# Performance work log

Hardware: AMD Instinct MI355X
Metric: run time of the kernel (lower is better)

The kernel has to match this reference:

```python
import jax, jax.numpy as jnp
import numpy as np

TOP_K_PCT = 0.1
MAX_SHARP_TOKENS = 10
SMOOTHING = 0.1


def setup_inputs() -> dict:
    key = jax.random.key(0)
    logits = jax.random.normal(key, (2, 8, 2048, 2048), dtype=jnp.float32)
    return {"logits": logits, "dim": 3}


def reference(logits, dim):
    # Move the softmax axis to the end so lax.top_k / row-scatter apply.
    x = jnp.moveaxis(logits, dim, -1)
    N = x.shape[-1]
    k = min(MAX_SHARP_TOKENS, max(1, int(N * TOP_K_PCT)))

    vals, idx = jax.lax.top_k(x, k)            # [..., k], sorted descending
    topk_soft = jax.nn.softmax(vals, axis=-1)  # softmax over just the top-k values

    flat = x.reshape(-1, N)                    # [R, N]
    fidx = idx.reshape(-1, k)                  # [R, k]
    rows = jnp.arange(flat.shape[0])[:, None]

    # boolean mask of top-k positions
    mask = jnp.zeros(flat.shape, dtype=bool).at[rows, fidx].set(True)

    # softmax over the remaining (non-top-k) logits; top-k filled with dtype min
    neg_inf = jnp.finfo(flat.dtype).min
    remaining = jnp.where(mask, neg_inf, flat)
    rem_soft = jax.nn.softmax(remaining, axis=-1)
    rem_soft = jnp.where(mask, jnp.zeros((), flat.dtype), rem_soft)

    # scatter top-k softmax back, then blend
    final = jnp.zeros_like(flat).at[rows, fidx].set(topk_soft.reshape(-1, k))
    out = final * (1.0 - SMOOTHING) + rem_soft * SMOOTHING

    return jnp.moveaxis(out.reshape(x.shape), -1, dim)
```

## Files before the change

### kernel.cpp

```cpp
#include <hip/hip_runtime.h>
#include <math.h>

#define ROW_N 2048
#define KSEL 10
#define WCAP 64

typedef float f32x4 __attribute__((ext_vector_type(4)));
typedef unsigned long long u64;

__global__ __launch_bounds__(256) void topk_softmax_kernel(
    const float* __restrict__ in, float* __restrict__ out)
{
    const int lane = threadIdx.x & 63;
    const int wave = threadIdx.x >> 6;
    const size_t base = ((size_t)blockIdx.x * 4 + wave) * ROW_N;

    __shared__ u64 s_cand[4][WCAP];

    const f32x4* p4 = reinterpret_cast<const f32x4*>(in + base);
    f32x4 V[8];
    #pragma unroll
    for (int j = 0; j < 8; ++j) V[j] = p4[j * 64 + lane];

    const float K = 1.4426950408889634f;
    float m1 = -INFINITY, m2 = -INFINITY, tot0 = 0.f;
    #pragma unroll
    for (int j = 0; j < 8; ++j)
        #pragma unroll
        for (int c = 0; c < 4; ++c) {
            float x = V[j][c];
            m2 = fmaxf(fminf(x, m1), m2);
            m1 = fmaxf(x, m1);
            tot0 += exp2f(x * K);
        }

    float vm = m1;
    #pragma unroll
    for (int off = 32; off > 0; off >>= 1) {
        vm = fmaxf(vm, __shfl_xor(vm, off));
        tot0 += __shfl_xor(tot0, off);
    }

    uint32_t u1 = __float_as_uint(m1);
    uint32_t u2 = __float_as_uint(m2);
    const uint32_t o1 = u1 ^ ((uint32_t)((int32_t)u1 >> 31) | 0x80000000u);
    const uint32_t o2 = u2 ^ ((uint32_t)((int32_t)u2 >> 31) | 0x80000000u);
    uint32_t kov = 0;
    #pragma unroll
    for (int b = 31; b >= 0; --b) {
        uint32_t t = kov | (1u << b);
        int cnt = __popcll(__ballot(o1 >= t)) + __popcll(__ballot(o2 >= t));
        if (cnt >= KSEL) kov = t;
    }
    const uint32_t kb = kov ^ ((kov & 0x80000000u) ? 0x80000000u : 0xFFFFFFFFu);
    const float kf = __uint_as_float(kb);

    int wc = 0;
    #pragma unroll
    for (int j = 0; j < 8; ++j)
        #pragma unroll
        for (int c = 0; c < 4; ++c) wc += (V[j][c] >= kf) ? 1 : 0;
    #pragma unroll
    for (int off = 32; off > 0; off >>= 1) wc += __shfl_xor(wc, off);

    const float c0v = -vm * K;
    const float tot = tot0 * exp2f(c0v);

    f32x4* o4 = reinterpret_cast<f32x4*>(out + base);

    if (wc == KSEL) {
        float e1 = (m1 >= kf) ? exp2f(fmaf(m1, K, c0v)) : 0.f;
        float e2 = (m2 >= kf) ? exp2f(fmaf(m2, K, c0v)) : 0.f;
        float ssum = e1 + e2;
        #pragma unroll
        for (int off = 32; off > 0; off >>= 1) ssum += __shfl_xor(ssum, off);

        const float aa = 0.9f / ssum;
        const float bb = 0.1f / (tot - ssum);
        #pragma unroll
        for (int j = 0; j < 8; ++j) {
            f32x4 o;
            #pragma unroll
            for (int c = 0; c < 4; ++c) {
                float x = V[j][c];
                float e = exp2f(fmaf(x, K, c0v));
                o[c] = e * ((x >= kf) ? aa : bb);
            }
            __builtin_nontemporal_store(o, o4 + j * 64 + lane);
        }
    } else {
        const int low0 = 2047 - lane * 4;
        int C = 0;
        #pragma unroll
        for (int j = 0; j < 8; ++j)
            #pragma unroll
            for (int c = 0; c < 4; ++c) {
                bool cond = V[j][c] >= kf;
                u64 m = __ballot(cond);
                if (cond) {
                    uint32_t u  = __float_as_uint(V[j][c]);
                    uint32_t ov = u ^ ((uint32_t)((int32_t)u >> 31) | 0x80000000u);
                    int pos = C + (int)__builtin_amdgcn_mbcnt_hi(
                                      (unsigned)(m >> 32),
                                      __builtin_amdgcn_mbcnt_lo((unsigned)m, 0u));
                    if (pos < WCAP)
                        s_cand[wave][pos] =
                            ((u64)ov << 16) | (unsigned)(low0 - (j * 256 + c));
                }
                C += __popcll(m);
            }
        if (C > WCAP) C = WCAP;

        u64 k0 = (lane < C) ? s_cand[wave][lane] : 0ULL;
        u64 kmin = 0ULL;
        #pragma unroll 1
        for (int b = 47; b >= 0; --b) {
            u64 trial = kmin | (1ULL << b);
            if (__popcll(__ballot(k0 >= trial)) >= KSEL) kmin = trial;
        }

        uint32_t ovk  = (uint32_t)(k0 >> 16);
        uint32_t bits = ovk ^ ((ovk & 0x80000000u) ? 0x80000000u : 0xFFFFFFFFu);
        float val = __uint_as_float(bits);
        bool win  = (k0 >= kmin) && (k0 != 0ULL);
        float ee  = win ? exp2f(fmaf(val, K, c0v)) : 0.f;
        float ssum = ee;
        #pragma unroll
        for (int off = 32; off > 0; off >>= 1) ssum += __shfl_xor(ssum, off);

        const float aa = 0.9f / ssum;
        const float bb = 0.1f / (tot - ssum);
        #pragma unroll
        for (int j = 0; j < 8; ++j) {
            f32x4 o;
            #pragma unroll
            for (int c = 0; c < 4; ++c) {
                float x = V[j][c];
                uint32_t u  = __float_as_uint(x);
                uint32_t ov = u ^ ((uint32_t)((int32_t)u >> 31) | 0x80000000u);
                u64 key = ((u64)ov << 16) | (unsigned)(low0 - (j * 256 + c));
                float e = exp2f(fmaf(x, K, c0v));
                o[c] = e * ((key >= kmin) ? aa : bb);
            }
            __builtin_nontemporal_store(o, o4 + j * 64 + lane);
        }
    }
}

extern "C" void kernel_launch(void* const* d_in, const int* in_sizes, int n_in,
                              void* d_out, int out_size, void* d_ws, size_t ws_size,
                              hipStream_t stream) {
    const float* logits = (const float*)d_in[0];
    float* out = (float*)d_out;
    const int rows = out_size / ROW_N;
    topk_softmax_kernel<<<dim3(rows / 4), dim3(256), 0, stream>>>(logits, out);
}
```

Before: 449.7 us.

## Process two rows per wave and replace the full count pass with a third-max check

Each wave now handles two rows and interleaves their loads, reductions and radix-select ballots, which raises instruction-level parallelism and halves the grid. The fast-path test no longer counts every element against the threshold. Instead it tracks a per-lane third maximum and checks that it stays below the threshold, while the top-k exponent sum is computed up front. The cost is doubled register use per thread (64 floats of row data), which may lower occupancy. The shared candidate buffer is also reused across the two emits with no barrier between them, which is fine within a single wave.

```diff
diff --git a/kernel.cpp b/kernel.cpp
--- a/kernel.cpp
+++ b/kernel.cpp
@@ -13,138 +13,159 @@
 {
     const int lane = threadIdx.x & 63;
     const int wave = threadIdx.x >> 6;
-    const size_t base = ((size_t)blockIdx.x * 4 + wave) * ROW_N;
+    const size_t baseA = ((size_t)blockIdx.x * 4 + wave) * 2 * ROW_N;
+    const size_t baseB = baseA + ROW_N;
 
     __shared__ u64 s_cand[4][WCAP];
 
-    const f32x4* p4 = reinterpret_cast<const f32x4*>(in + base);
-    f32x4 V[8];
+    const f32x4* pA = reinterpret_cast<const f32x4*>(in + baseA);
+    const f32x4* pB = reinterpret_cast<const f32x4*>(in + baseB);
+    f32x4 VA[8], VB[8];
     #pragma unroll
-    for (int j = 0; j < 8; ++j) V[j] = p4[j * 64 + lane];
+    for (int j = 0; j < 8; ++j) { VA[j] = pA[j * 64 + lane];
+                                  VB[j] = pB[j * 64 + lane]; }
 
     const float K = 1.4426950408889634f;
-    float m1 = -INFINITY, m2 = -INFINITY, tot0 = 0.f;
+    float a1 = -INFINITY, a2 = -INFINITY, a3 = -INFINITY, tA0 = 0.f;
+    float b1 = -INFINITY, b2 = -INFINITY, b3 = -INFINITY, tB0 = 0.f;
     #pragma unroll
     for (int j = 0; j < 8; ++j)
         #pragma unroll
         for (int c = 0; c < 4; ++c) {
-            float x = V[j][c];
-            m2 = fmaxf(fminf(x, m1), m2);
-            m1 = fmaxf(x, m1);
-            tot0 += exp2f(x * K);
+            float xA = VA[j][c];
+            a3 = fmaxf(fminf(xA, a2), a3);
+            a2 = fmaxf(fminf(xA, a1), a2);
+            a1 = fmaxf(xA, a1);
+            tA0 += exp2f(xA * K);
+            float xB = VB[j][c];
+            b3 = fmaxf(fminf(xB, b2), b3);
+            b2 = fmaxf(fminf(xB, b1), b2);
+            b1 = fmaxf(xB, b1);
+            tB0 += exp2f(xB * K);
         }
 
-    float vm = m1;
+    float vmA = a1, vmB = b1;
     #pragma unroll
     for (int off = 32; off > 0; off >>= 1) {
-        vm = fmaxf(vm, __shfl_xor(vm, off));
-        tot0 += __shfl_xor(tot0, off);
+        vmA = fmaxf(vmA, __shfl_xor(vmA, off));  tA0 += __shfl_xor(tA0, off);
+        vmB = fmaxf(vmB, __shfl_xor(vmB, off));  tB0 += __shfl_xor(tB0, off);
     }
 
-    uint32_t u1 = __float_as_uint(m1);
-    uint32_t u2 = __float_as_uint(m2);
-    const uint32_t o1 = u1 ^ ((uint32_t)((int32_t)u1 >> 31) | 0x80000000u);
-    const uint32_t o2 = u2 ^ ((uint32_t)((int32_t)u2 >> 31) | 0x80000000u);
-    uint32_t kov = 0;
+    auto ord = [](float x) {
+        uint32_t u = __float_as_uint(x);
+        return u ^ ((uint32_t)((int32_t)u >> 31) | 0x80000000u);
+    };
+    const uint32_t oa1 = ord(a1), oa2 = ord(a2);
+    const uint32_t ob1 = ord(b1), ob2 = ord(b2);
+
+    uint32_t kA = 0, kB = 0;
     #pragma unroll
     for (int b = 31; b >= 0; --b) {
-        uint32_t t = kov | (1u << b);
-        int cnt = __popcll(__ballot(o1 >= t)) + __popcll(__ballot(o2 >= t));
-        if (cnt >= KSEL) kov = t;
+        uint32_t tA = kA | (1u << b), tB = kB | (1u << b);
+        int cA = __popcll(__ballot(oa1 >= tA)) + __popcll(__ballot(oa2 >= tA));
+        int cB = __popcll(__ballot(ob1 >= tB)) + __popcll(__ballot(ob2 >= tB));
+        if (cA >= KSEL) kA = tA;
+        if (cB >= KSEL) kB = tB;
     }
-    const uint32_t kb = kov ^ ((kov & 0x80000000u) ? 0x80000000u : 0xFFFFFFFFu);
-    const float kf = __uint_as_float(kb);
+    auto unord = [](uint32_t o) {
+        return __uint_as_float(o ^ ((o & 0x80000000u) ? 0x80000000u
+                                                      : 0xFFFFFFFFu));
+    };
+    const float kfA = unord(kA), kfB = unord(kB);
 
-    int wc = 0;
+    int cA10 = __popcll(__ballot(oa1 >= kA)) + __popcll(__ballot(oa2 >= kA));
+    int cB10 = __popcll(__ballot(ob1 >= kB)) + __popcll(__ballot(ob2 >= kB));
+    const bool fastA = (cA10 == KSEL) && (__ballot(a3 >= kfA) == 0ULL);
+    const bool fastB = (cB10 == KSEL) && (__ballot(b3 >= kfB) == 0ULL);
+
+    const float c0A = -vmA * K, c0B = -vmB * K;
+    const float totA = tA0 * exp2f(c0A);
+    const float totB = tB0 * exp2f(c0B);
+
+    float eA = ((a1 >= kfA) ? exp2f(fmaf(a1, K, c0A)) : 0.f) +
+               ((a2 >= kfA) ? exp2f(fmaf(a2, K, c0A)) : 0.f);
+    float eB = ((b1 >= kfB) ? exp2f(fmaf(b1, K, c0B)) : 0.f) +
+               ((b2 >= kfB) ? exp2f(fmaf(b2, K, c0B)) : 0.f);
     #pragma unroll
-    for (int j = 0; j < 8; ++j)
-        #pragma unroll
-        for (int c = 0; c < 4; ++c) wc += (V[j][c] >= kf) ? 1 : 0;
-    #pragma unroll
-    for (int off = 32; off > 0; off >>= 1) wc += __shfl_xor(wc, off);
+    for (int off = 32; off > 0; off >>= 1) {
+        eA += __shfl_xor(eA, off);
+        eB += __shfl_xor(eB, off);
+    }
 
-    const float c0v = -vm * K;
-    const float tot = tot0 * exp2f(c0v);
+    const int low0 = 2047 - lane * 4;
 
-    f32x4* o4 = reinterpret_cast<f32x4*>(out + base);
+    auto emit = [&](f32x4 (&V)[8], size_t base, float kf, float c0v,
+                    float tot, float ssum, bool fast) {
+        f32x4* o4 = reinterpret_cast<f32x4*>(out + base);
+        if (fast) {
+            const float aa = 0.9f / ssum;
+            const float bb = 0.1f / (tot - ssum);
+            #pragma unroll
+            for (int j = 0; j < 8; ++j) {
+                f32x4 o;
+                #pragma unroll
+                for (int c = 0; c < 4; ++c) {
+                    float x = V[j][c];
+                    o[c] = exp2f(fmaf(x, K, c0v)) * ((x >= kf) ? aa : bb);
+                }
+                __builtin_nontemporal_store(o, o4 + j * 64 + lane);
+            }
+        } else {
+            int C = 0;
+            #pragma unroll
+            for (int j = 0; j < 8; ++j)
+                #pragma unroll
+                for (int c = 0; c < 4; ++c) {
+                    bool cond = V[j][c] >= kf;
+                    u64 m = __ballot(cond);
+                    if (cond) {
+                        uint32_t u  = __float_as_uint(V[j][c]);
+                        uint32_t ov = u ^ ((uint32_t)((int32_t)u >> 31) | 0x80000000u);
+                        int pos = C + (int)__builtin_amdgcn_mbcnt_hi(
+                                          (unsigned)(m >> 32),
+                                          __builtin_amdgcn_mbcnt_lo((unsigned)m, 0u));
+                        if (pos < WCAP)
+                            s_cand[wave][pos] =
+                                ((u64)ov << 16) | (unsigned)(low0 - (j * 256 + c));
+                    }
+                    C += __popcll(m);
+                }
+            if (C > WCAP) C = WCAP;
+            u64 k0 = (lane < C) ? s_cand[wave][lane] : 0ULL;
+            u64 kmin = 0ULL;
+            #pragma unroll 1
+            for (int b = 47; b >= 0; --b) {
+                u64 trial = kmin | (1ULL << b);
+                if (__popcll(__ballot(k0 >= trial)) >= KSEL) kmin = trial;
+            }
+            uint32_t ovk  = (uint32_t)(k0 >> 16);
+            uint32_t bits = ovk ^ ((ovk & 0x80000000u) ? 0x80000000u : 0xFFFFFFFFu);
+            float val = __uint_as_float(bits);
+            bool win  = (k0 >= kmin) && (k0 != 0ULL);
+            float ee  = win ? exp2f(fmaf(val, K, c0v)) : 0.f;
+            float ss = ee;
+            #pragma unroll
+            for (int off = 32; off > 0; off >>= 1) ss += __shfl_xor(ss, off);
+            const float aa = 0.9f / ss;
+            const float bb = 0.1f / (tot - ss);
+            #pragma unroll
+            for (int j = 0; j < 8; ++j) {
+                f32x4 o;
+                #pragma unroll
+                for (int c = 0; c < 4; ++c) {
+                    float x = V[j][c];
+                    uint32_t u  = __float_as_uint(x);
+                    uint32_t ov = u ^ ((uint32_t)((int32_t)u >> 31) | 0x80000000u);
+                    u64 key = ((u64)ov << 16) | (unsigned)(low0 - (j * 256 + c));
+                    o[c] = exp2f(fmaf(x, K, c0v)) * ((key >= kmin) ? aa : bb);
+                }
+                __builtin_nontemporal_store(o, o4 + j * 64 + lane);
+            }
+        }
+    };
 
-    if (wc == KSEL) {
-        float e1 = (m1 >= kf) ? exp2f(fmaf(m1, K, c0v)) : 0.f;
-        float e2 = (m2 >= kf) ? exp2f(fmaf(m2, K, c0v)) : 0.f;
-        float ssum = e1 + e2;
-        #pragma unroll
-        for (int off = 32; off > 0; off >>= 1) ssum += __shfl_xor(ssum, off);
-
-        const float aa = 0.9f / ssum;
-        const float bb = 0.1f / (tot - ssum);
-        #pragma unroll
-        for (int j = 0; j < 8; ++j) {
-            f32x4 o;
-            #pragma unroll
-            for (int c = 0; c < 4; ++c) {
-                float x = V[j][c];
-                float e = exp2f(fmaf(x, K, c0v));
-                o[c] = e * ((x >= kf) ? aa : bb);
-            }
-            __builtin_nontemporal_store(o, o4 + j * 64 + lane);
-        }
-    } else {
-        const int low0 = 2047 - lane * 4;
-        int C = 0;
-        #pragma unroll
-        for (int j = 0; j < 8; ++j)
-            #pragma unroll
-            for (int c = 0; c < 4; ++c) {
-                bool cond = V[j][c] >= kf;
-                u64 m = __ballot(cond);
-                if (cond) {
-                    uint32_t u  = __float_as_uint(V[j][c]);
-                    uint32_t ov = u ^ ((uint32_t)((int32_t)u >> 31) | 0x80000000u);
-                    int pos = C + (int)__builtin_amdgcn_mbcnt_hi(
-                                      (unsigned)(m >> 32),
-                                      __builtin_amdgcn_mbcnt_lo((unsigned)m, 0u));
-                    if (pos < WCAP)
-                        s_cand[wave][pos] =
-                            ((u64)ov << 16) | (unsigned)(low0 - (j * 256 + c));
-                }
-                C += __popcll(m);
-            }
-        if (C > WCAP) C = WCAP;
-
-        u64 k0 = (lane < C) ? s_cand[wave][lane] : 0ULL;
-        u64 kmin = 0ULL;
-        #pragma unroll 1
-        for (int b = 47; b >= 0; --b) {
-            u64 trial = kmin | (1ULL << b);
-            if (__popcll(__ballot(k0 >= trial)) >= KSEL) kmin = trial;
-        }
-
-        uint32_t ovk  = (uint32_t)(k0 >> 16);
-        uint32_t bits = ovk ^ ((ovk & 0x80000000u) ? 0x80000000u : 0xFFFFFFFFu);
-        float val = __uint_as_float(bits);
-        bool win  = (k0 >= kmin) && (k0 != 0ULL);
-        float ee  = win ? exp2f(fmaf(val, K, c0v)) : 0.f;
-        float ssum = ee;
-        #pragma unroll
-        for (int off = 32; off > 0; off >>= 1) ssum += __shfl_xor(ssum, off);
-
-        const float aa = 0.9f / ssum;
-        const float bb = 0.1f / (tot - ssum);
-        #pragma unroll
-        for (int j = 0; j < 8; ++j) {
-            f32x4 o;
-            #pragma unroll
-            for (int c = 0; c < 4; ++c) {
-                float x = V[j][c];
-                uint32_t u  = __float_as_uint(x);
-                uint32_t ov = u ^ ((uint32_t)((int32_t)u >> 31) | 0x80000000u);
-                u64 key = ((u64)ov << 16) | (unsigned)(low0 - (j * 256 + c));
-                float e = exp2f(fmaf(x, K, c0v));
-                o[c] = e * ((key >= kmin) ? aa : bb);
-            }
-            __builtin_nontemporal_store(o, o4 + j * 64 + lane);
-        }
-    }
+    emit(VA, baseA, kfA, c0A, totA, eA, fastA);
+    emit(VB, baseB, kfB, c0B, totB, eB, fastB);
 }
 
 extern "C" void kernel_launch(void* const* d_in, const int* in_sizes, int n_in,
@@ -153,5 +174,5 @@
     const float* logits = (const float*)d_in[0];
     float* out = (float*)d_out;
     const int rows = out_size / ROW_N;
-    topk_softmax_kernel<<<dim3(rows / 4), dim3(256), 0, stream>>>(logits, out);
+    topk_softmax_kernel<<<dim3(rows / 8), dim3(256), 0, stream>>>(logits, out);
 }
```

Result: faster. 434.9 us (-3.3%).

## Process eight rows per wave with double-buffered register prefetch

Applied to the files above, without the earlier changes.

Each wave now handles eight rows and loads the next row into a second register buffer while the current one is processed, so global loads overlap with compute. The threshold search takes two bits per step using three ballots at once, and the fast path now also checks a third per-lane maximum so the exact-ten case is confirmed without a full recount. In exchange the grid is eight times smaller and register pressure roughly doubles, which can lower occupancy.

```diff
diff --git a/kernel.cpp b/kernel.cpp
--- a/kernel.cpp
+++ b/kernel.cpp
@@ -4,146 +4,155 @@
 #define ROW_N 2048
 #define KSEL 10
 #define WCAP 64
+#define RPW  8
 
 typedef float f32x4 __attribute__((ext_vector_type(4)));
 typedef unsigned long long u64;
+
+__device__ __forceinline__ uint32_t ordbits(float x) {
+    uint32_t u = __float_as_uint(x);
+    return u ^ ((uint32_t)((int32_t)u >> 31) | 0x80000000u);
+}
+__device__ __forceinline__ float unord(uint32_t o) {
+    return __uint_as_float(o ^ ((o & 0x80000000u) ? 0x80000000u : 0xFFFFFFFFu));
+}
 
 __global__ __launch_bounds__(256) void topk_softmax_kernel(
     const float* __restrict__ in, float* __restrict__ out)
 {
     const int lane = threadIdx.x & 63;
     const int wave = threadIdx.x >> 6;
-    const size_t base = ((size_t)blockIdx.x * 4 + wave) * ROW_N;
+    const size_t row0 = ((size_t)blockIdx.x * 4 + wave) * RPW;
 
     __shared__ u64 s_cand[4][WCAP];
 
-    const f32x4* p4 = reinterpret_cast<const f32x4*>(in + base);
-    f32x4 V[8];
-    #pragma unroll
-    for (int j = 0; j < 8; ++j) V[j] = p4[j * 64 + lane];
+    const float K = 1.4426950408889634f;
+    const int low0 = 2047 - lane * 4;
 
-    const float K = 1.4426950408889634f;
-    float m1 = -INFINITY, m2 = -INFINITY, tot0 = 0.f;
-    #pragma unroll
-    for (int j = 0; j < 8; ++j)
+    f32x4 A[8], B[8];
+
+    auto loadrow = [&](f32x4 (&V)[8], size_t row) {
+        const f32x4* p = reinterpret_cast<const f32x4*>(in + row * ROW_N);
         #pragma unroll
-        for (int c = 0; c < 4; ++c) {
-            float x = V[j][c];
-            m2 = fmaxf(fminf(x, m1), m2);
-            m1 = fmaxf(x, m1);
-            tot0 += exp2f(x * K);
-        }
+        for (int j = 0; j < 8; ++j) V[j] = p[j * 64 + lane];
+    };
 
-    float vm = m1;
-    #pragma unroll
-    for (int off = 32; off > 0; off >>= 1) {
-        vm = fmaxf(vm, __shfl_xor(vm, off));
-        tot0 += __shfl_xor(tot0, off);
-    }
-
-    uint32_t u1 = __float_as_uint(m1);
-    uint32_t u2 = __float_as_uint(m2);
-    const uint32_t o1 = u1 ^ ((uint32_t)((int32_t)u1 >> 31) | 0x80000000u);
-    const uint32_t o2 = u2 ^ ((uint32_t)((int32_t)u2 >> 31) | 0x80000000u);
-    uint32_t kov = 0;
-    #pragma unroll
-    for (int b = 31; b >= 0; --b) {
-        uint32_t t = kov | (1u << b);
-        int cnt = __popcll(__ballot(o1 >= t)) + __popcll(__ballot(o2 >= t));
-        if (cnt >= KSEL) kov = t;
-    }
-    const uint32_t kb = kov ^ ((kov & 0x80000000u) ? 0x80000000u : 0xFFFFFFFFu);
-    const float kf = __uint_as_float(kb);
-
-    int wc = 0;
-    #pragma unroll
-    for (int j = 0; j < 8; ++j)
-        #pragma unroll
-        for (int c = 0; c < 4; ++c) wc += (V[j][c] >= kf) ? 1 : 0;
-    #pragma unroll
-    for (int off = 32; off > 0; off >>= 1) wc += __shfl_xor(wc, off);
-
-    const float c0v = -vm * K;
-    const float tot = tot0 * exp2f(c0v);
-
-    f32x4* o4 = reinterpret_cast<f32x4*>(out + base);
-
-    if (wc == KSEL) {
-        float e1 = (m1 >= kf) ? exp2f(fmaf(m1, K, c0v)) : 0.f;
-        float e2 = (m2 >= kf) ? exp2f(fmaf(m2, K, c0v)) : 0.f;
-        float ssum = e1 + e2;
-        #pragma unroll
-        for (int off = 32; off > 0; off >>= 1) ssum += __shfl_xor(ssum, off);
-
-        const float aa = 0.9f / ssum;
-        const float bb = 0.1f / (tot - ssum);
-        #pragma unroll
-        for (int j = 0; j < 8; ++j) {
-            f32x4 o;
-            #pragma unroll
-            for (int c = 0; c < 4; ++c) {
-                float x = V[j][c];
-                float e = exp2f(fmaf(x, K, c0v));
-                o[c] = e * ((x >= kf) ? aa : bb);
-            }
-            __builtin_nontemporal_store(o, o4 + j * 64 + lane);
-        }
-    } else {
-        const int low0 = 2047 - lane * 4;
-        int C = 0;
+    auto process = [&](f32x4 (&V)[8], size_t row) {
+        float m1 = -INFINITY, m2 = -INFINITY, m3 = -INFINITY, t0 = 0.f;
         #pragma unroll
         for (int j = 0; j < 8; ++j)
             #pragma unroll
             for (int c = 0; c < 4; ++c) {
-                bool cond = V[j][c] >= kf;
-                u64 m = __ballot(cond);
-                if (cond) {
-                    uint32_t u  = __float_as_uint(V[j][c]);
-                    uint32_t ov = u ^ ((uint32_t)((int32_t)u >> 31) | 0x80000000u);
-                    int pos = C + (int)__builtin_amdgcn_mbcnt_hi(
-                                      (unsigned)(m >> 32),
-                                      __builtin_amdgcn_mbcnt_lo((unsigned)m, 0u));
-                    if (pos < WCAP)
-                        s_cand[wave][pos] =
-                            ((u64)ov << 16) | (unsigned)(low0 - (j * 256 + c));
-                }
-                C += __popcll(m);
+                float x = V[j][c];
+                m3 = fmaxf(fminf(x, m2), m3);
+                m2 = fmaxf(fminf(x, m1), m2);
+                m1 = fmaxf(x, m1);
+                t0 += exp2f(x * K);
             }
-        if (C > WCAP) C = WCAP;
 
-        u64 k0 = (lane < C) ? s_cand[wave][lane] : 0ULL;
-        u64 kmin = 0ULL;
-        #pragma unroll 1
-        for (int b = 47; b >= 0; --b) {
-            u64 trial = kmin | (1ULL << b);
-            if (__popcll(__ballot(k0 >= trial)) >= KSEL) kmin = trial;
+        float vm = m1;
+        #pragma unroll
+        for (int off = 32; off > 0; off >>= 1) {
+            vm = fmaxf(vm, __shfl_xor(vm, off));
+            t0 += __shfl_xor(t0, off);
         }
 
-        uint32_t ovk  = (uint32_t)(k0 >> 16);
-        uint32_t bits = ovk ^ ((ovk & 0x80000000u) ? 0x80000000u : 0xFFFFFFFFu);
-        float val = __uint_as_float(bits);
-        bool win  = (k0 >= kmin) && (k0 != 0ULL);
-        float ee  = win ? exp2f(fmaf(val, K, c0v)) : 0.f;
-        float ssum = ee;
+        const uint32_t o1 = ordbits(m1), o2 = ordbits(m2);
+        auto cnt = [&](uint32_t t) {
+            return __popcll(__ballot(o1 >= t)) + __popcll(__ballot(o2 >= t));
+        };
+
+        uint32_t kov = 0;
         #pragma unroll
-        for (int off = 32; off > 0; off >>= 1) ssum += __shfl_xor(ssum, off);
+        for (int b = 30; b >= 0; b -= 2) {
+            uint32_t t3 = kov | (3u << b), t2 = kov | (2u << b), t1 = kov | (1u << b);
+            int c3 = cnt(t3), c2 = cnt(t2), c1 = cnt(t1);
+            kov = (c3 >= KSEL) ? t3 : (c2 >= KSEL) ? t2 : (c1 >= KSEL) ? t1 : kov;
+        }
+        const float kf = unord(kov);
 
-        const float aa = 0.9f / ssum;
-        const float bb = 0.1f / (tot - ssum);
-        #pragma unroll
-        for (int j = 0; j < 8; ++j) {
-            f32x4 o;
+        const bool fast = (cnt(kov) == KSEL) && (__ballot(m3 >= kf) == 0ULL);
+        const float c0v = -vm * K;
+        const float tot = t0 * exp2f(c0v);
+
+        f32x4* o4 = reinterpret_cast<f32x4*>(out + row * ROW_N);
+
+        if (fast) {
+            float ee = ((m1 >= kf) ? exp2f(fmaf(m1, K, c0v)) : 0.f) +
+                       ((m2 >= kf) ? exp2f(fmaf(m2, K, c0v)) : 0.f);
             #pragma unroll
-            for (int c = 0; c < 4; ++c) {
-                float x = V[j][c];
-                uint32_t u  = __float_as_uint(x);
-                uint32_t ov = u ^ ((uint32_t)((int32_t)u >> 31) | 0x80000000u);
-                u64 key = ((u64)ov << 16) | (unsigned)(low0 - (j * 256 + c));
-                float e = exp2f(fmaf(x, K, c0v));
-                o[c] = e * ((key >= kmin) ? aa : bb);
+            for (int off = 32; off > 0; off >>= 1) ee += __shfl_xor(ee, off);
+            const float aa = 0.9f / ee;
+            const float bb = 0.1f / (tot - ee);
+            #pragma unroll
+            for (int j = 0; j < 8; ++j) {
+                f32x4 o;
+                #pragma unroll
+                for (int c = 0; c < 4; ++c) {
+                    float x = V[j][c];
+                    o[c] = exp2f(fmaf(x, K, c0v)) * ((x >= kf) ? aa : bb);
+                }
+                __builtin_nontemporal_store(o, o4 + j * 64 + lane);
             }
-            __builtin_nontemporal_store(o, o4 + j * 64 + lane);
+        } else {
+            int C = 0;
+            #pragma unroll
+            for (int j = 0; j < 8; ++j)
+                #pragma unroll
+                for (int c = 0; c < 4; ++c) {
+                    bool cond = V[j][c] >= kf;
+                    u64 m = __ballot(cond);
+                    if (cond) {
+                        int pos = C + (int)__builtin_amdgcn_mbcnt_hi(
+                                          (unsigned)(m >> 32),
+                                          __builtin_amdgcn_mbcnt_lo((unsigned)m, 0u));
+                        if (pos < WCAP)
+                            s_cand[wave][pos] = ((u64)ordbits(V[j][c]) << 16) |
+                                                (unsigned)(low0 - (j * 256 + c));
+                    }
+                    C += __popcll(m);
+                }
+            if (C > WCAP) C = WCAP;
+            u64 k0 = (lane < C) ? s_cand[wave][lane] : 0ULL;
+            u64 kmin = 0ULL;
+            #pragma unroll 1
+            for (int b = 47; b >= 0; --b) {
+                u64 trial = kmin | (1ULL << b);
+                if (__popcll(__ballot(k0 >= trial)) >= KSEL) kmin = trial;
+            }
+            uint32_t ovk = (uint32_t)(k0 >> 16);
+            float val = unord(ovk);
+            bool win  = (k0 >= kmin) && (k0 != 0ULL);
+            float ee  = win ? exp2f(fmaf(val, K, c0v)) : 0.f;
+            float ss = ee;
+            #pragma unroll
+            for (int off = 32; off > 0; off >>= 1) ss += __shfl_xor(ss, off);
+            const float aa = 0.9f / ss;
+            const float bb = 0.1f / (tot - ss);
+            #pragma unroll
+            for (int j = 0; j < 8; ++j) {
+                f32x4 o;
+                #pragma unroll
+                for (int c = 0; c < 4; ++c) {
+                    float x = V[j][c];
+                    u64 key = ((u64)ordbits(x) << 16) |
+                              (unsigned)(low0 - (j * 256 + c));
+                    o[c] = exp2f(fmaf(x, K, c0v)) * ((key >= kmin) ? aa : bb);
+                }
+                __builtin_nontemporal_store(o, o4 + j * 64 + lane);
+            }
         }
+    };
+
+    loadrow(A, row0);
+    #pragma unroll 1
+    for (int i = 0; i < RPW; i += 2) {
+        loadrow(B, row0 + i + 1);
+        asm volatile("" ::: "memory");
+        process(A, row0 + i);
+        if (i + 2 < RPW) loadrow(A, row0 + i + 2);
+        asm volatile("" ::: "memory");
+        process(B, row0 + i + 1);
     }
 }
 
@@ -153,5 +162,6 @@
     const float* logits = (const float*)d_in[0];
     float* out = (float*)d_out;
     const int rows = out_size / ROW_N;
-    topk_softmax_kernel<<<dim3(rows / 4), dim3(256), 0, stream>>>(logits, out);
+    const int waves = rows / RPW;
+    topk_softmax_kernel<<<dim3(waves / 4), dim3(256), 0, stream>>>(logits, out);
 }
```

After: 460.7 us. +2.4%, slower.
